# Optimization experiments

Hardware: AMD Instinct MI355X
Metric: run time of the kernel (lower is better)

## Reference

```python
import jax, jax.numpy as jnp
import numpy as np
import math

B, L, H = 2, 2048, 2048
NH, HD, RD = 16, 128, 64
QR, KVR = 768, 512


def rotate_half(x):
    d = x.shape[-1]
    x1, x2 = x[..., : d // 2], x[..., d // 2 :]
    return jnp.concatenate([-x2, x1], axis=-1)


def apply_rope(x):
    # x: [B, L, H, D] or [B, L, D]
    d = x.shape[-1]
    seq_len = x.shape[1]
    inv_freq = 1.0 / (10000.0 ** (jnp.arange(0, d, 2, dtype=x.dtype) / d))
    pos = jnp.arange(seq_len, dtype=x.dtype)
    freqs = jnp.outer(pos, inv_freq)  # [L, d/2]
    cos = jnp.concatenate([jnp.cos(freqs), jnp.cos(freqs)], axis=-1)  # [L, d]
    sin = jnp.concatenate([jnp.sin(freqs), jnp.sin(freqs)], axis=-1)
    if x.ndim == 4:
        cos, sin = cos[None, :, None, :], sin[None, :, None, :]
    else:
        cos, sin = cos[None, :, :], sin[None, :, :]
    return x * cos + rotate_half(x) * sin


def setup_inputs() -> dict:
    key = jax.random.key(0)
    ks = jax.random.split(key, 9)
    sc = lambda fan_in: 1.0 / math.sqrt(fan_in)
    return {
        "x": jax.random.normal(ks[0], (B, L, H), jnp.float32),
        "wq_down": jax.random.normal(ks[1], (H, QR), jnp.float32) * sc(H),
        "wq_up": jax.random.normal(ks[2], (QR, NH * HD), jnp.float32) * sc(QR),
        "wq_rope": jax.random.normal(ks[3], (QR, NH * RD), jnp.float32) * sc(QR),
        "wkv_down": jax.random.normal(ks[4], (H, KVR), jnp.float32) * sc(H),
        "wk_up": jax.random.normal(ks[5], (KVR, NH * HD), jnp.float32) * sc(KVR),
        "wv_up": jax.random.normal(ks[6], (KVR, NH * HD), jnp.float32) * sc(KVR),
        "wk_rope": jax.random.normal(ks[7], (H, RD), jnp.float32) * sc(H),
        "wo": jax.random.normal(ks[8], (NH * HD, H), jnp.float32) * sc(NH * HD),
    }


def reference(x, wq_down, wq_up, wq_rope, wkv_down, wk_up, wv_up, wk_rope, wo):
    b, l, _ = x.shape
    # Q low-rank path
    q_latent = x @ wq_down                              # [B,L,QR]
    q_content = (q_latent @ wq_up).reshape(b, l, NH, HD)
    q_rope = (q_latent @ wq_rope).reshape(b, l, NH, RD)
    q_rope = apply_rope(q_rope)
    # KV joint low-rank path
    kv_latent = x @ wkv_down                            # [B,L,KVR]
    k_content = (kv_latent @ wk_up).reshape(b, l, NH, HD)
    v = (kv_latent @ wv_up).reshape(b, l, NH, HD)
    # decoupled RoPE key (shared across heads)
    k_rope = apply_rope(x @ wk_rope)                    # [B,L,RD]
    k_rope = jnp.broadcast_to(k_rope[:, :, None, :], (b, l, NH, RD))
    q = jnp.concatenate([q_content, q_rope], axis=-1)   # [B,L,NH,HD+RD]
    k = jnp.concatenate([k_content, k_rope], axis=-1)
    scale = 1.0 / math.sqrt(HD + RD)
    scores = jnp.einsum("bqhd,bkhd->bhqk", q, k) * scale
    causal_mask = jnp.triu(jnp.ones((l, l), dtype=bool), k=1)
    scores = jnp.where(causal_mask[None, None], -jnp.inf, scores)
    attn = jax.nn.softmax(scores, axis=-1)
    out = jnp.einsum("bhqk,bkhd->bqhd", attn, v).reshape(b, l, NH * HD)
    return out @ wo
```

## Files before the change

kernel.cpp:

```cpp
#include <hip/hip_runtime.h>

typedef unsigned short u16;
typedef unsigned int u32;
typedef unsigned long long u64;
typedef __bf16 bf16x8 __attribute__((ext_vector_type(8)));
typedef float f32x4 __attribute__((ext_vector_type(4)));
typedef float f32x16 __attribute__((ext_vector_type(16)));
typedef u32 u32x4 __attribute__((ext_vector_type(4)));

#define DEV static __device__ __forceinline__

constexpr int B_ = 2, L_ = 2048, H_ = 2048;
constexpr int NH_ = 16, HD_ = 128, RD_ = 64;
constexpr int QR_ = 768, KVR_ = 512;
constexpr int BL_ = B_ * L_;
constexpr int QKD_ = HD_ + RD_;
constexpr int QKS_ = NH_ * QKD_;
constexpr int NHHD_ = NH_ * HD_;
constexpr int ROWS_ = B_ * NH_ * L_;
constexpr float SCALE2 = 0.07216878364870322f * 1.4426950408889634f;

DEV u16 f2bf(float f) {
    __bf16 h = (__bf16)f;
    return __builtin_bit_cast(u16, h);
}
DEV float bf2f(u16 h) {
    u32 u = ((u32)h) << 16;
    return __builtin_bit_cast(float, u);
}
DEV u32 pk2(float lo, float hi) { return (u32)f2bf(lo) | ((u32)f2bf(hi) << 16); }
DEV bf16x8 ld8(const u16* p) { return __builtin_bit_cast(bf16x8, *(const u32x4*)p); }
DEV f32x4 mfma16(bf16x8 a, bf16x8 b, f32x4 c) {
    return __builtin_amdgcn_mfma_f32_16x16x32_bf16(a, b, c, 0, 0, 0);
}
DEV f32x16 mfma32(bf16x8 a, bf16x8 b, f32x16 c) {
    return __builtin_amdgcn_mfma_f32_32x32x16_bf16(a, b, c, 0, 0, 0);
}
DEV void gload16(const void* g, void* l) {
    __builtin_amdgcn_global_load_lds((const __attribute__((address_space(1))) void*)g,
                                     (__attribute__((address_space(3))) void*)l, 16, 0, 0);
}
DEV void plswap(u32& a, u32& b) {
    asm("v_permlane32_swap_b32 %0, %1" : "+v"(a), "+v"(b));
}

__global__ __launch_bounds__(256) void cast_bf16_kernel(const float* __restrict__ src,
                                                        u16* __restrict__ dst, int n4) {
    int i = blockIdx.x * 256 + threadIdx.x;
    if (i >= n4) return;
    float4 v = ((const float4*)src)[i];
    u64 pk = (u64)f2bf(v.x) | ((u64)f2bf(v.y) << 16) | ((u64)f2bf(v.z) << 32) | ((u64)f2bf(v.w) << 48);
    ((u64*)dst)[i] = pk;
}

__global__ __launch_bounds__(256) void transpose_all(
    const float* __restrict__ s0, const float* __restrict__ s1, const float* __restrict__ s2,
    const float* __restrict__ s3, const float* __restrict__ s4, const float* __restrict__ s5,
    const float* __restrict__ s6, const float* __restrict__ s7,
    u16* __restrict__ Wdn, u16* __restrict__ Wupq, u16* __restrict__ Wupkv, u16* __restrict__ Wo_t) {
    int t = blockIdx.x;
    const float* src; u16* dst; int K, N, nx;
    if (t < 1536)       {            src = s0; dst = Wdn;                          K = 2048; N = 768;  nx = 24; }
    else if (t < 2560)  { t -= 1536; src = s1; dst = Wdn + (size_t)768 * 2048;     K = 2048; N = 512;  nx = 16; }
    else if (t < 2816)  { t -= 2560; src = s2; dst = Wdn + (size_t)1280 * 2048;    K = 2048; N = 64;   nx = 4;  }
    else if (t < 4352)  { t -= 2816; src = s3; dst = Wupq;                         K = 768;  N = 2048; nx = 64; }
    else if (t < 5120)  { t -= 4352; src = s4; dst = Wupq + (size_t)2048 * 768;    K = 768;  N = 1024; nx = 32; }
    else if (t < 6144)  { t -= 5120; src = s5; dst = Wupkv;                        K = 512;  N = 2048; nx = 64; }
    else if (t < 7168)  { t -= 6144; src = s6; dst = Wupkv + (size_t)2048 * 512;   K = 512;  N = 2048; nx = 64; }
    else                { t -= 7168; src = s7; dst = Wo_t;                         K = 2048; N = 2048; nx = 64; }
    const int n0 = (t % nx) * 32, k0 = (t / nx) * 32;

    __shared__ float tile[32][33];
    int tx = threadIdx.x & 31, ty = threadIdx.x >> 5;
#pragma unroll
    for (int i = 0; i < 4; ++i) {
        int kk = ty + i * 8;
        int n = n0 + tx;
        tile[kk][tx] = (n < N) ? src[(size_t)(k0 + kk) * N + n] : 0.f;
    }
    __syncthreads();
#pragma unroll
    for (int i = 0; i < 4; ++i) {
        int nn = ty + i * 8;
        dst[(size_t)(n0 + nn) * K + k0 + tx] = f2bf(tile[tx][nn]);
    }
}

__global__ __launch_bounds__(256) void build_rope_tab(float2* __restrict__ tab) {
    int idx = blockIdx.x * 256 + threadIdx.x;
    int pos = idx >> 5, i = idx & 31;
    float freq = exp2f((float)i * (-13.287712379549449f / 32.f));
    float ang = (float)pos * freq;
    tab[idx] = make_float2(cosf(ang), sinf(ang));
}

template <int EPI>
__global__ __launch_bounds__(256, 2) void gemm_bt(const u16* __restrict__ A, int lda,
                                                  const u16* __restrict__ Bt,
                                                  void* __restrict__ Cv, void* __restrict__ Cv2,
                                                  int ldc, int K, const float2* __restrict__ tab) {
    __shared__ u16 As[128 * 64];
    __shared__ u16 Bs[128 * 64];
    const int tid = threadIdx.x;
    const int l = tid & 63, w = tid >> 6;
    const int l15 = l & 15, g = l >> 4;
    const int wr = w >> 1, wc = w & 1;
    const int NX = gridDim.x;
    const int fid = blockIdx.x + NX * blockIdx.y;
    const int G = (NX * gridDim.y) >> 3;
    const int lin = (fid & 7) * G + (fid >> 3);
    const int bm = (lin / NX) * 128, bn = (lin % NX) * 128;

    const f32x4 zero = {0.f, 0.f, 0.f, 0.f};
    f32x4 acc[4][4];
#pragma unroll
    for (int m = 0; m < 4; ++m)
#pragma unroll
        for (int n = 0; n < 4; ++n) acc[m][n] = zero;

    int aoff[4], boff[4];
#pragma unroll
    for (int j = 0; j < 4; ++j) {
        int chunk = j * 256 + tid;
        int row = chunk >> 3, gr = chunk & 7;
        aoff[j] = row * lda + gr * 8;
        boff[j] = row * K + gr * 8;
    }
    const u16* Ab = A + (size_t)bm * lda;
    const u16* Bb = Bt + (size_t)bn * K;

    const int nK = K / 64;
    for (int kt = 0; kt < nK; ++kt) {
        const int ko = kt * 64;
        __syncthreads();
#pragma unroll
        for (int j = 0; j < 4; ++j) gload16(Ab + ko + aoff[j], As + j * 2048 + w * 512);
#pragma unroll
        for (int j = 0; j < 4; ++j) gload16(Bb + ko + boff[j], Bs + j * 2048 + w * 512);
        __syncthreads();
#pragma unroll
        for (int kk = 0; kk < 2; ++kk) {
            bf16x8 af[4], bfr[4];
#pragma unroll
            for (int m = 0; m < 4; ++m)
                af[m] = ld8(As + (wr * 64 + m * 16 + l15) * 64 + kk * 32 + g * 8);
#pragma unroll
            for (int n = 0; n < 4; ++n)
                bfr[n] = ld8(Bs + (wc * 64 + n * 16 + l15) * 64 + kk * 32 + g * 8);
#pragma unroll
            for (int m = 0; m < 4; ++m)
#pragma unroll
                for (int n = 0; n < 4; ++n) acc[m][n] = mfma16(af[m], bfr[n], acc[m][n]);
        }
    }

    if constexpr (EPI == 0 || EPI == 1) {
#pragma unroll
        for (int m = 0; m < 4; ++m)
#pragma unroll
            for (int n = 0; n < 4; ++n)
#pragma unroll
                for (int r = 0; r < 4; ++r) {
                    int row = bm + wr * 64 + m * 16 + g * 4 + r;
                    int col = bn + wc * 64 + n * 16 + l15;
                    if (EPI == 1)
                        ((float*)Cv)[(size_t)row * ldc + col] = acc[m][n][r];
                    else
                        ((u16*)Cv)[(size_t)row * ldc + col] = f2bf(acc[m][n][r]);
                }
    }
    if constexpr (EPI == 2) {
        const int base = bn + wc * 64;
        u16* qb = (u16*)Cv;
        if (base < 2048) {
            const int h = base >> 7, dbase = base & 127;
#pragma unroll
            for (int m = 0; m < 4; ++m)
#pragma unroll
                for (int n = 0; n < 4; ++n)
#pragma unroll
                    for (int r = 0; r < 4; ++r) {
                        int token = bm + wr * 64 + m * 16 + g * 4 + r;
                        qb[(size_t)token * QKS_ + h * QKD_ + dbase + n * 16 + l15] =
                            f2bf(acc[m][n][r] * SCALE2);
                    }
        } else {
            const int h = (base - 2048) >> 6;
#pragma unroll
            for (int m = 0; m < 4; ++m)
#pragma unroll
                for (int r = 0; r < 4; ++r) {
                    const int token = bm + wr * 64 + m * 16 + g * 4 + r;
                    const int pos = token & (L_ - 1);
                    u16* bp = qb + (size_t)token * QKS_ + h * QKD_ + HD_;
#pragma unroll
                    for (int n = 0; n < 2; ++n) {
                        const int i = n * 16 + l15;
                        float2 cs = tab[pos * 32 + i];
                        float x1 = acc[m][n][r], x2 = acc[m][n + 2][r];
                        bp[i] = f2bf((x1 * cs.x - x2 * cs.y) * SCALE2);
                        bp[i + 32] = f2bf((x2 * cs.x + x1 * cs.y) * SCALE2);
                    }
                }
        }
    }
    if constexpr (EPI == 3) {
        const int base = bn + wc * 64;
        if (base < 2048) {
            u16* kb = (u16*)Cv;
            const int h = base >> 7, dbase = base & 127;
#pragma unroll
            for (int m = 0; m < 4; ++m)
#pragma unroll
                for (int n = 0; n < 4; ++n)
#pragma unroll
                    for (int r = 0; r < 4; ++r) {
                        int token = bm + wr * 64 + m * 16 + g * 4 + r;
                        kb[(size_t)token * QKS_ + h * QKD_ + dbase + n * 16 + l15] =
                            f2bf(acc[m][n][r]);
                    }
        } else {
            u16* vtb = (u16*)Cv2;
            const int b = bm >> 11;
#pragma unroll
            for (int m = 0; m < 4; ++m)
#pragma unroll
                for (int n = 0; n < 4; ++n) {
                    const int vc = base - 2048 + n * 16 + l15;
                    const int qrow = (bm + wr * 64 + m * 16 + g * 4) & (L_ - 1);
                    u64 pk = (u64)pk2(acc[m][n][0], acc[m][n][1]) |
                             ((u64)pk2(acc[m][n][2], acc[m][n][3]) << 32);
                    *(u64*)(vtb + (size_t)(b * NHHD_ + vc) * L_ + qrow) = pk;
                }
        }
    }
}

__global__ __launch_bounds__(256) void rope_k_kernel(const u16* __restrict__ src, int S,
                                                     u16* __restrict__ dst,
                                                     const float2* __restrict__ tab) {
    int idx = blockIdx.x * 256 + threadIdx.x;
    int token = idx >> 5, i = idx & 31;
    int pos = token & (L_ - 1);
    float2 cs = tab[pos * 32 + i];
    float x1 = bf2f(src[(size_t)token * S + i]);
    float x2 = bf2f(src[(size_t)token * S + i + 32]);
    u16 o1 = f2bf(x1 * cs.x - x2 * cs.y);
    u16 o2 = f2bf(x2 * cs.x + x1 * cs.y);
    u16* base = dst + (size_t)token * QKS_ + HD_;
#pragma unroll
    for (int h = 0; h < NH_; ++h) {
        base[h * QKD_ + i] = o1;
        base[h * QKD_ + i + 32] = o2;
    }
}

__global__ __launch_bounds__(256, 2) void flash_attn(const u16* __restrict__ q, const u16* __restrict__ k,
                                                     const u16* __restrict__ vt,
                                                     u16* __restrict__ opart, float* __restrict__ mlpart) {
    __shared__ __align__(16) u16 Ks[2][64 * 192];
    __shared__ __align__(16) u16 Vs[2][128 * 64];
    const int fid = blockIdx.x + 16 * blockIdx.y + 256 * blockIdx.z;
    const int xcd = fid & 7, slot = fid >> 3;
    const int group = xcd * 4 + (slot >> 4);
    const int member = slot & 15;
    const int b = group >> 4, h = group & 15;
    const int p = member >> 1, split = member & 1;
    const int tid = threadIdx.x, w = tid >> 6, l = tid & 63;
    const int ql = l & 31, hi = l >> 5;
    const int sw = ql & 7;

    const u16* kbase = k + (size_t)(b * L_) * QKS_ + h * QKD_;
    const u16* vtbase = vt + (size_t)(b * NHHD_ + h * HD_) * L_;

    int koff[6], voff[4];
#pragma unroll
    for (int j = 0; j < 6; ++j) {
        int off = j * 4096 + tid * 16;
        int row = off / 384;
        int gr = (off % 384) / 16;
        koff[j] = row * QKS_ + (gr ^ (row & 7)) * 8;
    }
#pragma unroll
    for (int j = 0; j < 4; ++j) {
        int off = j * 4096 + tid * 16;
        int row = off >> 7;
        int gr = (off >> 4) & 7;
        voff[j] = row * L_ + (gr ^ (row & 7)) * 8;
    }

    auto STAGE = [&](int buf, int kv0) {
        const u16* kb = kbase + (size_t)kv0 * QKS_;
#pragma unroll
        for (int j = 0; j < 6; ++j)
            gload16(kb + koff[j], (u16*)Ks[buf] + j * 2048 + w * 512);
        const u16* vb = vtbase + kv0;
#pragma unroll
        for (int j = 0; j < 4; ++j)
            gload16(vb + voff[j], (u16*)Vs[buf] + j * 2048 + w * 512);
    };

    for (int half = 0; half < 2; ++half) {
        const int qtile = half ? 15 - p : p;
        const int q0 = qtile * 128;
        const int qabs = q0 + w * 32 + ql;

        bf16x8 qf[12];
        {
            const u16* qrow = q + (size_t)(b * L_ + qabs) * QKS_ + h * QKD_;
#pragma unroll
            for (int c = 0; c < 12; ++c) qf[c] = ld8(qrow + c * 16 + hi * 8);
        }
        f32x16 o[4];
#pragma unroll
        for (int n = 0; n < 4; ++n)
#pragma unroll
            for (int r = 0; r < 16; ++r) o[n][r] = 0.f;
        float m2 = -1e30f, lsum = 0.f;

        const int nt = 2 * qtile + 2;
        __syncthreads();
        STAGE(0, split * 64);
        int i = 0;
        for (int t = split; t < nt; t += 2, ++i) {
            __syncthreads();
            if (t + 2 < nt) STAGE((i + 1) & 1, (t + 2) * 64);
            const u16* Kb = Ks[i & 1];
            const u16* Vb = Vs[i & 1];
            const int kv0 = t * 64;

            f32x16 s0, s1;
#pragma unroll
            for (int r = 0; r < 16; ++r) { s0[r] = 0.f; s1[r] = 0.f; }
#pragma unroll
            for (int c = 0; c < 12; ++c) {
                int gsw = ((2 * c + hi) ^ sw) * 16;
                bf16x8 k0 = ld8((const u16*)((const char*)Kb + ql * 384 + gsw));
                bf16x8 k1 = ld8((const u16*)((const char*)Kb + (32 + ql) * 384 + gsw));
                s0 = mfma32(k0, qf[c], s0);
                s1 = mfma32(k1, qf[c], s1);
            }

            const bool domask = (kv0 + 63 > q0);
            float mx = -3e38f;
#pragma unroll
            for (int r = 0; r < 16; ++r) {
                const int kk = (r & 3) + 8 * (r >> 2) + 4 * hi;
                float x0 = s0[r];
                float x1 = s1[r];
                if (domask) {
                    if (kv0 + kk > qabs) x0 = -3e38f;
                    if (kv0 + 32 + kk > qabs) x1 = -3e38f;
                }
                s0[r] = x0; s1[r] = x1;
                mx = fmaxf(mx, fmaxf(x0, x1));
            }
            mx = fmaxf(mx, __shfl_xor(mx, 32));

            if (__any(mx > m2 + 8.f)) {
                const float mnew = fmaxf(m2, mx);
                const float f = exp2f(m2 - mnew);
                m2 = mnew;
                lsum *= f;
#pragma unroll
                for (int n = 0; n < 4; ++n)
#pragma unroll
                    for (int r = 0; r < 16; ++r) o[n][r] *= f;
            }

            float sl = 0.f;
#pragma unroll
            for (int r = 0; r < 16; ++r) {
                float p0 = exp2f(s0[r] - m2);
                float p1 = exp2f(s1[r] - m2);
                s0[r] = p0; s1[r] = p1;
                sl += p0 + p1;
            }
            lsum += sl;

#pragma unroll
            for (int c = 0; c < 4; ++c) {
                const int rb = 8 * (c & 1);
                float p0, p1, p2, p3, p4, p5, p6, p7;
                if (c < 2) {
                    p0 = s0[rb + 0]; p1 = s0[rb + 1]; p2 = s0[rb + 2]; p3 = s0[rb + 3];
                    p4 = s0[rb + 4]; p5 = s0[rb + 5]; p6 = s0[rb + 6]; p7 = s0[rb + 7];
                } else {
                    p0 = s1[rb + 0]; p1 = s1[rb + 1]; p2 = s1[rb + 2]; p3 = s1[rb + 3];
                    p4 = s1[rb + 4]; p5 = s1[rb + 5]; p6 = s1[rb + 6]; p7 = s1[rb + 7];
                }
                u32 a0 = pk2(p0, p1), a1 = pk2(p2, p3);
                u32 b0 = pk2(p4, p5), b1 = pk2(p6, p7);
                plswap(a0, b0);
                plswap(a1, b1);
                u32x4 pw = {a0, a1, b0, b1};
                bf16x8 pf = __builtin_bit_cast(bf16x8, pw);
                const int gsw = ((2 * c + hi) ^ sw) * 16;
#pragma unroll
                for (int n = 0; n < 4; ++n) {
                    bf16x8 vf = ld8((const u16*)((const char*)Vb + (32 * n + ql) * 128 + gsw));
                    o[n] = mfma32(vf, pf, o[n]);
                }
            }
        }

        const float ltot = lsum + __shfl_xor(lsum, 32);
        const int row = ((b * NH_ + h) << 11) + qabs;
        u16* ob = opart + ((size_t)split * ROWS_ + row) * 128;
#pragma unroll
        for (int n = 0; n < 4; ++n)
#pragma unroll
            for (int rg = 0; rg < 4; ++rg) {
                const int d0 = 32 * n + 8 * rg + 4 * hi;
                u64 pk = (u64)pk2(o[n][4 * rg + 0], o[n][4 * rg + 1]) |
                         ((u64)pk2(o[n][4 * rg + 2], o[n][4 * rg + 3]) << 32);
                *(u64*)(ob + d0) = pk;
            }
        if (!hi) {
            float2 ml = {m2, ltot};
            *(float2*)(mlpart + ((size_t)split * ROWS_ + row) * 2) = ml;
        }
    }
}

__global__ __launch_bounds__(256) void combine_attn(const u16* __restrict__ opart,
                                                    const float* __restrict__ mlpart,
                                                    u16* __restrict__ attn_o) {
    int idx = blockIdx.x * 256 + threadIdx.x;
    int row = idx >> 5, dq = (idx & 31) * 4;
    float2 ml0 = *(const float2*)(mlpart + (size_t)row * 2);
    float2 ml1 = *(const float2*)(mlpart + ((size_t)ROWS_ + row) * 2);
    float m = fmaxf(ml0.x, ml1.x);
    float w0 = exp2f(ml0.x - m), w1 = exp2f(ml1.x - m);
    float inv = 1.f / (w0 * ml0.y + w1 * ml1.y);
    w0 *= inv; w1 *= inv;
    u64 av = *(const u64*)(opart + (size_t)row * 128 + dq);
    u64 cv = *(const u64*)(opart + ((size_t)ROWS_ + row) * 128 + dq);
    float a0 = bf2f((u16)av), a1 = bf2f((u16)(av >> 16));
    float a2 = bf2f((u16)(av >> 32)), a3 = bf2f((u16)(av >> 48));
    float c0 = bf2f((u16)cv), c1 = bf2f((u16)(cv >> 16));
    float c2 = bf2f((u16)(cv >> 32)), c3 = bf2f((u16)(cv >> 48));
    int b = row >> 15, h = (row >> 11) & 15, qrow = row & 2047;
    u16* dst = attn_o + (size_t)(b * L_ + qrow) * NHHD_ + h * HD_ + dq;
    u64 pk = (u64)pk2(a0 * w0 + c0 * w1, a1 * w0 + c1 * w1) |
             ((u64)pk2(a2 * w0 + c2 * w1, a3 * w0 + c3 * w1) << 32);
    *(u64*)dst = pk;
}

extern "C" void kernel_launch(void* const* d_in, const int* in_sizes, int n_in,
                              void* d_out, int out_size, void* d_ws, size_t ws_size,
                              hipStream_t stream) {
    (void)in_sizes; (void)n_in; (void)out_size; (void)ws_size;
    const float* x = (const float*)d_in[0];
    const float* wq_down = (const float*)d_in[1];
    const float* wq_up = (const float*)d_in[2];
    const float* wq_rope = (const float*)d_in[3];
    const float* wkv_down = (const float*)d_in[4];
    const float* wk_up = (const float*)d_in[5];
    const float* wv_up = (const float*)d_in[6];
    const float* wk_rope = (const float*)d_in[7];
    const float* wo = (const float*)d_in[8];

    u16* W = (u16*)d_ws;
    size_t off = 0;
    auto alloc = [&](size_t e) { u16* p = W + off; off += (e + 127) & ~(size_t)127; return p; };

    u16* xb    = alloc((size_t)BL_ * H_);
    u16* Wdn   = alloc((size_t)1408 * H_);
    u16* Wupq  = alloc((size_t)3072 * QR_);
    u16* Wupkv = alloc((size_t)4096 * KVR_);
    u16* Wo_t  = alloc((size_t)H_ * NHHD_);
    u16* tabm  = alloc((size_t)L_ * 32 * 4);
    u16* C1    = alloc((size_t)BL_ * 1408);
    u16* pad_  = alloc((size_t)28311552);
    u16* qbuf  = alloc((size_t)BL_ * QKS_);
    u16* kbuf  = alloc((size_t)BL_ * QKS_);
    u16* vt    = alloc((size_t)BL_ * NHHD_);
    u16* attn_o = alloc((size_t)BL_ * NHHD_);
    (void)pad_;

    float2* tab = (float2*)tabm;
    u16* opart    = C1;
    float* mlpart = (float*)(C1 + (size_t)2 * ROWS_ * 128);

    cast_bf16_kernel<<<(BL_ * H_ / 4 + 255) / 256, 256, 0, stream>>>(x, xb, BL_ * H_ / 4);
    transpose_all<<<11264, 256, 0, stream>>>(wq_down, wkv_down, wk_rope, wq_up, wq_rope,
                                             wk_up, wv_up, wo, Wdn, Wupq, Wupkv, Wo_t);
    build_rope_tab<<<L_ * 32 / 256, 256, 0, stream>>>(tab);

    gemm_bt<0><<<dim3(1408 / 128, BL_ / 128), 256, 0, stream>>>(xb, H_, Wdn, C1, nullptr, 1408, H_, nullptr);
    gemm_bt<2><<<dim3(3072 / 128, BL_ / 128), 256, 0, stream>>>(C1, 1408, Wupq, qbuf, nullptr, 0, QR_, tab);
    gemm_bt<3><<<dim3(4096 / 128, BL_ / 128), 256, 0, stream>>>(C1 + 768, 1408, Wupkv, kbuf, vt, 0, KVR_, nullptr);

    rope_k_kernel<<<BL_ * 32 / 256, 256, 0, stream>>>(C1 + 1280, 1408, kbuf, tab);

    flash_attn<<<dim3(16, NH_, B_), 256, 0, stream>>>(qbuf, kbuf, vt, opart, mlpart);
    combine_attn<<<ROWS_ * 32 / 256, 256, 0, stream>>>(opart, mlpart, attn_o);

    gemm_bt<1><<<dim3(H_ / 128, BL_ / 128), 256, 0, stream>>>(attn_o, NHHD_, Wo_t, d_out, nullptr, H_, NHHD_, nullptr);
}
```

Baseline: 273.2 us.

## Split flash attention KV range four ways with 32-wide KV tiles

```diff
diff --git a/kernel.cpp b/kernel.cpp
--- a/kernel.cpp
+++ b/kernel.cpp
@@ -255,48 +255,49 @@
     }
 }
 
-__global__ __launch_bounds__(256, 2) void flash_attn(const u16* __restrict__ q, const u16* __restrict__ k,
+__global__ __launch_bounds__(256, 4) void flash_attn(const u16* __restrict__ q, const u16* __restrict__ k,
                                                      const u16* __restrict__ vt,
                                                      u16* __restrict__ opart, float* __restrict__ mlpart) {
-    __shared__ __align__(16) u16 Ks[2][64 * 192];
-    __shared__ __align__(16) u16 Vs[2][128 * 64];
-    const int fid = blockIdx.x + 16 * blockIdx.y + 256 * blockIdx.z;
+    __shared__ __align__(16) u16 Ks[2][32 * 192];
+    __shared__ __align__(16) u16 Vs[2][128 * 32];
+    const int fid = blockIdx.x + 32 * blockIdx.y + 512 * blockIdx.z;
     const int xcd = fid & 7, slot = fid >> 3;
-    const int group = xcd * 4 + (slot >> 4);
-    const int member = slot & 15;
+    const int group = xcd * 4 + (slot >> 5);
+    const int member = slot & 31;
     const int b = group >> 4, h = group & 15;
-    const int p = member >> 1, split = member & 1;
+    const int p = member >> 2, split = member & 3;
     const int tid = threadIdx.x, w = tid >> 6, l = tid & 63;
     const int ql = l & 31, hi = l >> 5;
     const int sw = ql & 7;
+    const int swv = (ql >> 1) & 3;
 
     const u16* kbase = k + (size_t)(b * L_) * QKS_ + h * QKD_;
     const u16* vtbase = vt + (size_t)(b * NHHD_ + h * HD_) * L_;
 
-    int koff[6], voff[4];
-#pragma unroll
-    for (int j = 0; j < 6; ++j) {
+    int koff[3], voff[2];
+#pragma unroll
+    for (int j = 0; j < 3; ++j) {
         int off = j * 4096 + tid * 16;
         int row = off / 384;
         int gr = (off % 384) / 16;
         koff[j] = row * QKS_ + (gr ^ (row & 7)) * 8;
     }
 #pragma unroll
-    for (int j = 0; j < 4; ++j) {
+    for (int j = 0; j < 2; ++j) {
         int off = j * 4096 + tid * 16;
-        int row = off >> 7;
-        int gr = (off >> 4) & 7;
-        voff[j] = row * L_ + (gr ^ (row & 7)) * 8;
+        int row = off >> 6;
+        int gr = (off >> 4) & 3;
+        voff[j] = row * L_ + (gr ^ ((row >> 1) & 3)) * 8;
     }
 
     auto STAGE = [&](int buf, int kv0) {
         const u16* kb = kbase + (size_t)kv0 * QKS_;
 #pragma unroll
-        for (int j = 0; j < 6; ++j)
+        for (int j = 0; j < 3; ++j)
             gload16(kb + koff[j], (u16*)Ks[buf] + j * 2048 + w * 512);
         const u16* vb = vtbase + kv0;
 #pragma unroll
-        for (int j = 0; j < 4; ++j)
+        for (int j = 0; j < 2; ++j)
             gload16(vb + voff[j], (u16*)Vs[buf] + j * 2048 + w * 512);
     };
 
@@ -318,42 +319,36 @@
             for (int r = 0; r < 16; ++r) o[n][r] = 0.f;
         float m2 = -1e30f, lsum = 0.f;
 
-        const int nt = 2 * qtile + 2;
+        const int ntk = 4 * qtile + 4;
         __syncthreads();
-        STAGE(0, split * 64);
+        STAGE(0, split * 32);
         int i = 0;
-        for (int t = split; t < nt; t += 2, ++i) {
+        for (int t = split; t < ntk; t += 4, ++i) {
             __syncthreads();
-            if (t + 2 < nt) STAGE((i + 1) & 1, (t + 2) * 64);
+            if (t + 4 < ntk) STAGE((i + 1) & 1, (t + 4) * 32);
             const u16* Kb = Ks[i & 1];
             const u16* Vb = Vs[i & 1];
-            const int kv0 = t * 64;
-
-            f32x16 s0, s1;
-#pragma unroll
-            for (int r = 0; r < 16; ++r) { s0[r] = 0.f; s1[r] = 0.f; }
+            const int kv0 = t * 32;
+
+            f32x16 s0;
+#pragma unroll
+            for (int r = 0; r < 16; ++r) s0[r] = 0.f;
 #pragma unroll
             for (int c = 0; c < 12; ++c) {
                 int gsw = ((2 * c + hi) ^ sw) * 16;
                 bf16x8 k0 = ld8((const u16*)((const char*)Kb + ql * 384 + gsw));
-                bf16x8 k1 = ld8((const u16*)((const char*)Kb + (32 + ql) * 384 + gsw));
                 s0 = mfma32(k0, qf[c], s0);
-                s1 = mfma32(k1, qf[c], s1);
-            }
-
-            const bool domask = (kv0 + 63 > q0);
+            }
+
+            const bool domask = (kv0 + 31 > q0);
             float mx = -3e38f;
 #pragma unroll
             for (int r = 0; r < 16; ++r) {
                 const int kk = (r & 3) + 8 * (r >> 2) + 4 * hi;
                 float x0 = s0[r];
-                float x1 = s1[r];
-                if (domask) {
-                    if (kv0 + kk > qabs) x0 = -3e38f;
-                    if (kv0 + 32 + kk > qabs) x1 = -3e38f;
-                }
-                s0[r] = x0; s1[r] = x1;
-                mx = fmaxf(mx, fmaxf(x0, x1));
+                if (domask && (kv0 + kk > qabs)) x0 = -3e38f;
+                s0[r] = x0;
+                mx = fmaxf(mx, x0);
             }
             mx = fmaxf(mx, __shfl_xor(mx, 32));
 
@@ -372,33 +367,26 @@
 #pragma unroll
             for (int r = 0; r < 16; ++r) {
                 float p0 = exp2f(s0[r] - m2);
-                float p1 = exp2f(s1[r] - m2);
-                s0[r] = p0; s1[r] = p1;
-                sl += p0 + p1;
+                s0[r] = p0;
+                sl += p0;
             }
             lsum += sl;
 
 #pragma unroll
-            for (int c = 0; c < 4; ++c) {
-                const int rb = 8 * (c & 1);
-                float p0, p1, p2, p3, p4, p5, p6, p7;
-                if (c < 2) {
-                    p0 = s0[rb + 0]; p1 = s0[rb + 1]; p2 = s0[rb + 2]; p3 = s0[rb + 3];
-                    p4 = s0[rb + 4]; p5 = s0[rb + 5]; p6 = s0[rb + 6]; p7 = s0[rb + 7];
-                } else {
-                    p0 = s1[rb + 0]; p1 = s1[rb + 1]; p2 = s1[rb + 2]; p3 = s1[rb + 3];
-                    p4 = s1[rb + 4]; p5 = s1[rb + 5]; p6 = s1[rb + 6]; p7 = s1[rb + 7];
-                }
-                u32 a0 = pk2(p0, p1), a1 = pk2(p2, p3);
-                u32 b0 = pk2(p4, p5), b1 = pk2(p6, p7);
+            for (int c = 0; c < 2; ++c) {
+                const int rb = 8 * c;
+                u32 a0 = pk2(s0[rb + 0], s0[rb + 1]);
+                u32 a1 = pk2(s0[rb + 2], s0[rb + 3]);
+                u32 b0 = pk2(s0[rb + 4], s0[rb + 5]);
+                u32 b1 = pk2(s0[rb + 6], s0[rb + 7]);
                 plswap(a0, b0);
                 plswap(a1, b1);
                 u32x4 pw = {a0, a1, b0, b1};
                 bf16x8 pf = __builtin_bit_cast(bf16x8, pw);
-                const int gsw = ((2 * c + hi) ^ sw) * 16;
+                const int gsv = ((2 * c + hi) ^ swv) * 16;
 #pragma unroll
                 for (int n = 0; n < 4; ++n) {
-                    bf16x8 vf = ld8((const u16*)((const char*)Vb + (32 * n + ql) * 128 + gsw));
+                    bf16x8 vf = ld8((const u16*)((const char*)Vb + (32 * n + ql) * 64 + gsv));
                     o[n] = mfma32(vf, pf, o[n]);
                 }
             }
@@ -428,22 +416,32 @@
                                                     u16* __restrict__ attn_o) {
     int idx = blockIdx.x * 256 + threadIdx.x;
     int row = idx >> 5, dq = (idx & 31) * 4;
-    float2 ml0 = *(const float2*)(mlpart + (size_t)row * 2);
-    float2 ml1 = *(const float2*)(mlpart + ((size_t)ROWS_ + row) * 2);
-    float m = fmaxf(ml0.x, ml1.x);
-    float w0 = exp2f(ml0.x - m), w1 = exp2f(ml1.x - m);
-    float inv = 1.f / (w0 * ml0.y + w1 * ml1.y);
-    w0 *= inv; w1 *= inv;
-    u64 av = *(const u64*)(opart + (size_t)row * 128 + dq);
-    u64 cv = *(const u64*)(opart + ((size_t)ROWS_ + row) * 128 + dq);
-    float a0 = bf2f((u16)av), a1 = bf2f((u16)(av >> 16));
-    float a2 = bf2f((u16)(av >> 32)), a3 = bf2f((u16)(av >> 48));
-    float c0 = bf2f((u16)cv), c1 = bf2f((u16)(cv >> 16));
-    float c2 = bf2f((u16)(cv >> 32)), c3 = bf2f((u16)(cv >> 48));
+    float2 ml[4];
+    float m = -3e38f;
+#pragma unroll
+    for (int s = 0; s < 4; ++s) {
+        ml[s] = *(const float2*)(mlpart + ((size_t)s * ROWS_ + row) * 2);
+        m = fmaxf(m, ml[s].x);
+    }
+    float wgt[4], denom = 0.f;
+#pragma unroll
+    for (int s = 0; s < 4; ++s) {
+        wgt[s] = exp2f(ml[s].x - m);
+        denom += wgt[s] * ml[s].y;
+    }
+    const float inv = 1.f / denom;
+    float acc0 = 0.f, acc1 = 0.f, acc2 = 0.f, acc3 = 0.f;
+#pragma unroll
+    for (int s = 0; s < 4; ++s) {
+        u64 v = *(const u64*)(opart + ((size_t)s * ROWS_ + row) * 128 + dq);
+        acc0 += bf2f((u16)v) * wgt[s];
+        acc1 += bf2f((u16)(v >> 16)) * wgt[s];
+        acc2 += bf2f((u16)(v >> 32)) * wgt[s];
+        acc3 += bf2f((u16)(v >> 48)) * wgt[s];
+    }
     int b = row >> 15, h = (row >> 11) & 15, qrow = row & 2047;
     u16* dst = attn_o + (size_t)(b * L_ + qrow) * NHHD_ + h * HD_ + dq;
-    u64 pk = (u64)pk2(a0 * w0 + c0 * w1, a1 * w0 + c1 * w1) |
-             ((u64)pk2(a2 * w0 + c2 * w1, a3 * w0 + c3 * w1) << 32);
+    u64 pk = (u64)pk2(acc0 * inv, acc1 * inv) | ((u64)pk2(acc2 * inv, acc3 * inv) << 32);
     *(u64*)dst = pk;
 }
 
@@ -472,7 +470,7 @@
     u16* Wo_t  = alloc((size_t)H_ * NHHD_);
     u16* tabm  = alloc((size_t)L_ * 32 * 4);
     u16* C1    = alloc((size_t)BL_ * 1408);
-    u16* pad_  = alloc((size_t)28311552);
+    u16* pad_  = alloc((size_t)28835840);
     u16* qbuf  = alloc((size_t)BL_ * QKS_);
     u16* kbuf  = alloc((size_t)BL_ * QKS_);
     u16* vt    = alloc((size_t)BL_ * NHHD_);
@@ -481,7 +479,7 @@
 
     float2* tab = (float2*)tabm;
     u16* opart    = C1;
-    float* mlpart = (float*)(C1 + (size_t)2 * ROWS_ * 128);
+    float* mlpart = (float*)(C1 + (size_t)4 * ROWS_ * 128);
 
     cast_bf16_kernel<<<(BL_ * H_ / 4 + 255) / 256, 256, 0, stream>>>(x, xb, BL_ * H_ / 4);
     transpose_all<<<11264, 256, 0, stream>>>(wq_down, wkv_down, wk_rope, wq_up, wq_rope,
@@ -494,7 +492,7 @@
 
     rope_k_kernel<<<BL_ * 32 / 256, 256, 0, stream>>>(C1 + 1280, 1408, kbuf, tab);
 
-    flash_attn<<<dim3(16, NH_, B_), 256, 0, stream>>>(qbuf, kbuf, vt, opart, mlpart);
+    flash_attn<<<dim3(32, NH_, B_), 256, 0, stream>>>(qbuf, kbuf, vt, opart, mlpart);
     combine_attn<<<ROWS_ * 32 / 256, 256, 0, stream>>>(opart, mlpart, attn_o);
 
     gemm_bt<1><<<dim3(H_ / 128, BL_ / 128), 256, 0, stream>>>(attn_o, NHHD_, Wo_t, d_out, nullptr, H_, NHHD_, nullptr);
```

Result: slower. 431.1 us (+57.8%).
